# Kernel optimization log

Measured on AMD Instinct MI355X. Metric: run time of the kernel, lower is better.

Reference implementation:

```python
import jax, jax.numpy as jnp
import numpy as np

VOCAB = 50257
H = 512  # output_size == embed dim == lstm hidden
N = 65536  # number of tokens


def setup_inputs() -> dict:
    key = jax.random.key(0)
    ks = jax.random.split(key, 12)
    s = 1.0 / np.sqrt(H)  # torch LSTM/Linear init scale
    inp = {
        "ids": jax.random.randint(ks[0], (N,), 0, VOCAB, dtype=jnp.int64)
        if jax.config.jax_enable_x64 else jax.random.randint(ks[0], (N,), 0, VOCAB, dtype=jnp.int32),
        "emb": jax.random.normal(ks[1], (VOCAB, H), dtype=jnp.float32),
        # LSTM layer 0 (gate order: i, f, g, o)
        "W_ih0": jax.random.uniform(ks[2], (4 * H, H), jnp.float32, -s, s),
        "W_hh0": jax.random.uniform(ks[3], (4 * H, H), jnp.float32, -s, s),
        "b_ih0": jax.random.uniform(ks[4], (4 * H,), jnp.float32, -s, s),
        "b_hh0": jax.random.uniform(ks[5], (4 * H,), jnp.float32, -s, s),
        # LSTM layer 1
        "W_ih1": jax.random.uniform(ks[6], (4 * H, H), jnp.float32, -s, s),
        "W_hh1": jax.random.uniform(ks[7], (4 * H, H), jnp.float32, -s, s),
        "b_ih1": jax.random.uniform(ks[8], (4 * H,), jnp.float32, -s, s),
        "b_hh1": jax.random.uniform(ks[9], (4 * H,), jnp.float32, -s, s),
        # final Linear
        "W_lin": jax.random.uniform(ks[10], (H, H), jnp.float32, -s, s),
        "b_lin": jax.random.uniform(ks[11], (H,), jnp.float32, -s, s),
    }
    return inp


def _lstm_cell_zero_state(x, W_ih, b_ih, b_hh):
    # Single LSTM step with h_prev = c_prev = 0, so W_hh @ h_prev == 0.
    # gates: [N, 4H] in torch order i, f, g, o
    gates = x @ W_ih.T + (b_ih + b_hh)
    i, f, g, o = jnp.split(gates, 4, axis=-1)
    c = jax.nn.sigmoid(i) * jnp.tanh(g)  # f * c_prev == 0
    h = jax.nn.sigmoid(o) * jnp.tanh(c)
    return h


def reference(ids, emb, W_ih0, W_hh0, b_ih0, b_hh0, W_ih1, W_hh1, b_ih1, b_hh1, W_lin, b_lin):
    # Each token is processed with a fresh zero LSTM state, so the python
    # loop in the original vectorizes exactly over the token dim.
    x = emb[ids]                                   # [N, H]
    h0 = _lstm_cell_zero_state(x, W_ih0, b_ih0, b_hh0)   # layer 1 hidden
    h1 = _lstm_cell_zero_state(h0, W_ih1, b_ih1, b_hh1)  # layer 2 hidden (hidden[-1])
    out = jax.nn.relu(h1 @ W_lin.T + b_lin)        # [N, H]
    return out[:, None, :]                         # stacked [N, 1, H] like torch.stack of [1,H]
```

## Files before the change

kernel.cpp:

```cpp
#include <hip/hip_runtime.h>
#include <stdint.h>


typedef _Float16 half8 __attribute__((ext_vector_type(8)));
typedef __attribute__((ext_vector_type(4))) float float4v;
typedef __attribute__((ext_vector_type(4))) unsigned int uint4v;

__device__ __forceinline__ float sigmoidf_(float x) { return 1.0f / (1.0f + __expf(-x)); }
__device__ __forceinline__ float tanhf_(float x) { return 1.0f - 2.0f / (__expf(2.0f * x) + 1.0f); }

__device__ __forceinline__ void gl2lds16(const void* g, void* l) {
  __builtin_amdgcn_global_load_lds(
      (const __attribute__((address_space(1))) void*)g,
      (__attribute__((address_space(3))) void*)l, 16, 0, 0);
}

__global__ __launch_bounds__(256) void prep_kernel(
    const float* __restrict__ emb,
    const float* __restrict__ W0, const float* __restrict__ bi0, const float* __restrict__ bh0,
    const float* __restrict__ W1, const float* __restrict__ bi1, const float* __restrict__ bh1,
    const float* __restrict__ WL,
    _Float16* __restrict__ Ef,
    _Float16* __restrict__ W0f, _Float16* __restrict__ W1f, _Float16* __restrict__ WLf,
    float* __restrict__ b0p, float* __restrict__ b1p)
{
  int id = blockIdx.x * 256 + threadIdx.x;
  if (id < 3216448) {
    const float* s = emb + (size_t)id * 8;
    float4v v0 = *(const float4v*)s;
    float4v v1 = *(const float4v*)(s + 4);
    union { _Float16 h[8]; uint4v u; } P;
#pragma unroll
    for (int e = 0; e < 4; ++e) { P.h[e] = (_Float16)v0[e]; P.h[4 + e] = (_Float16)v1[e]; }
    *(uint4v*)(Ef + (size_t)id * 8) = P.u;
  } else if (id < 3347520) {
    int u = id - 3216448;
    int np = u >> 6, k0 = (u & 63) << 3;
    int n = ((np & 3) << 9) | (np >> 2);
    const float* s = W0 + n * 512 + k0;
    float4v v0 = *(const float4v*)s;
    float4v v1 = *(const float4v*)(s + 4);
    union { _Float16 h[8]; uint4v u; } P;
#pragma unroll
    for (int e = 0; e < 4; ++e) { P.h[e] = (_Float16)v0[e]; P.h[4 + e] = (_Float16)v1[e]; }
    *(uint4v*)(W0f + np * 512 + k0) = P.u;
  } else if (id < 3478592) {
    int u = id - 3347520;
    int np = u >> 6, k0 = (u & 63) << 3;
    int n = ((np & 3) << 9) | (np >> 2);
    const float* s = W1 + n * 512 + k0;
    float4v v0 = *(const float4v*)s;
    float4v v1 = *(const float4v*)(s + 4);
    union { _Float16 h[8]; uint4v u; } P;
#pragma unroll
    for (int e = 0; e < 4; ++e) { P.h[e] = (_Float16)v0[e]; P.h[4 + e] = (_Float16)v1[e]; }
    *(uint4v*)(W1f + np * 512 + k0) = P.u;
  } else if (id < 3511360) {
    int u = id - 3478592;
    const float* s = WL + (size_t)u * 8;
    float4v v0 = *(const float4v*)s;
    float4v v1 = *(const float4v*)(s + 4);
    union { _Float16 h[8]; uint4v u8; } P;
#pragma unroll
    for (int e = 0; e < 4; ++e) { P.h[e] = (_Float16)v0[e]; P.h[4 + e] = (_Float16)v1[e]; }
    *(uint4v*)(WLf + (size_t)u * 8) = P.u8;
  } else if (id < 3513408) {
    int np = id - 3511360;
    int n = ((np & 3) << 9) | (np >> 2);
    b0p[np] = bi0[n] + bh0[n];
  } else if (id < 3515456) {
    int np = id - 3513408;
    int n = ((np & 3) << 9) | (np >> 2);
    b1p[np] = bi1[n] + bh1[n];
  } else if (id < 3526656) {
    int u = id - 3515456;
    *(uint4v*)(Ef + 25731584 + (size_t)u * 8) = (uint4v){0u, 0u, 0u, 0u};
  }
}

template <int MODE>
__global__ __launch_bounds__(512, 4) void gemm_kernel(
    const _Float16* __restrict__ A, const int* __restrict__ ids,
    const _Float16* __restrict__ B, const float* __restrict__ bias,
    _Float16* __restrict__ Of, float* __restrict__ Out,
    int nbShift, int nbMask)
{
  __shared__ __align__(16) char smem[24576];
  _Float16* sA = (_Float16*)smem;
  _Float16* sB = (_Float16*)(smem + 16384);

  const int T = threadIdx.x;
  const int lane = T & 63;
  const int wv = T >> 6;
  const int wrow = wv >> 1, wcol = wv & 1;
  const int nwg = (int)gridDim.x;
  const int bid = (int)blockIdx.x;
  const int swz = (bid & 7) * (nwg >> 3) + (bid >> 3);
  const int mb = swz >> nbShift;
  const int nb = swz & nbMask;
  const size_t t0 = (size_t)mb * 256;
  const int n0 = nb * 128;

  const int r0 = T >> 2;
  const int qg = (T & 3) ^ ((r0 >> 1) & 3);
  size_t sr0 = t0 + r0, sr1 = t0 + 128 + r0;
  if (ids) { sr0 = (size_t)(unsigned)ids[sr0]; sr1 = (size_t)(unsigned)ids[sr1]; }
  const _Float16* gA0 = A + sr0 * 512 + qg * 8;
  const _Float16* gA1 = A + sr1 * 512 + qg * 8;
  const _Float16* gB  = B + (size_t)(n0 + r0) * 512 + qg * 8;

  const int m_ = lane & 15, qf = lane >> 4;
  const int qs = qf ^ ((m_ >> 1) & 3);
  const int offA = wrow * 2048 + m_ * 32 + qs * 8;
  const int offB = wcol * 2048 + m_ * 32 + qs * 8;

  float4v acc[4][4];
#pragma unroll
  for (int i = 0; i < 4; ++i)
#pragma unroll
    for (int j = 0; j < 4; ++j)
      acc[i][j] = (float4v){0.f, 0.f, 0.f, 0.f};

  for (int it = 0; it < 16; ++it) {
    gl2lds16(gA0, sA + T * 8);
    gl2lds16(gA1, sA + 4096 + T * 8);
    gl2lds16(gB,  sB + T * 8);
    gA0 += 32; gA1 += 32; gB += 32;
    __syncthreads();

    half8 a[4], b[4];
#pragma unroll
    for (int i = 0; i < 4; ++i) {
      a[i] = *(const half8*)(sA + offA + i * 512);
      b[i] = *(const half8*)(sB + offB + i * 512);
    }
#pragma unroll
    for (int i = 0; i < 4; ++i)
#pragma unroll
      for (int j = 0; j < 4; ++j)
        acc[i][j] = __builtin_amdgcn_mfma_f32_16x16x32_f16(b[j], a[i], acc[i][j], 0, 0, 0);
    __syncthreads();
  }

  float4v bq[4];
#pragma unroll
  for (int j = 0; j < 4; ++j)
    bq[j] = *(const float4v*)(bias + n0 + wcol * 64 + j * 16 + qf * 4);

  if (MODE == 0) {
    _Float16* hT = (_Float16*)smem;
    const int ub = wcol * 16 + qf;
#pragma unroll
    for (int i = 0; i < 4; ++i) {
      const int trow = wrow * 64 + i * 16 + m_;
#pragma unroll
      for (int j = 0; j < 4; ++j) {
        float yi = acc[i][j][0] + bq[j][0];
        float yg = acc[i][j][2] + bq[j][2];
        float yo = acc[i][j][3] + bq[j][3];
        float cc = sigmoidf_(yi) * tanhf_(yg);
        float hh = sigmoidf_(yo) * tanhf_(cc);
        hT[trow * 40 + ub + j * 4] = (_Float16)hh;
      }
    }
    __syncthreads();
    const int tl = T >> 1, hf = T & 1;
    const _Float16* src = hT + tl * 40 + hf * 16;
    uint4v v0 = *(const uint4v*)(src);
    uint4v v1 = *(const uint4v*)(src + 8);
    _Float16* dst = Of + (t0 + tl) * 512 + (size_t)(nb * 32) + hf * 16;
    *(uint4v*)dst = v0;
    *(uint4v*)(dst + 8) = v1;
  } else {
#pragma unroll
    for (int i = 0; i < 4; ++i) {
      const size_t row = t0 + wrow * 64 + i * 16 + m_;
#pragma unroll
      for (int j = 0; j < 4; ++j) {
        float4v v;
#pragma unroll
        for (int r2 = 0; r2 < 4; ++r2)
          v[r2] = fmaxf(acc[i][j][r2] + bq[j][r2], 0.0f);
        *(float4v*)(Out + row * 512 + (size_t)(n0 + wcol * 64 + j * 16 + qf * 4)) = v;
      }
    }
  }
}

extern "C" void kernel_launch(void* const* d_in, const int* in_sizes, int n_in,
                              void* d_out, int out_size, void* d_ws, size_t ws_size,
                              hipStream_t stream) {
  (void)in_sizes; (void)n_in; (void)out_size; (void)ws_size;
  const int*   ids   = (const int*)d_in[0];
  const float* emb   = (const float*)d_in[1];
  const float* W0    = (const float*)d_in[2];
  const float* bi0   = (const float*)d_in[4];
  const float* bh0   = (const float*)d_in[5];
  const float* W1    = (const float*)d_in[6];
  const float* bi1   = (const float*)d_in[8];
  const float* bh1   = (const float*)d_in[9];
  const float* WL    = (const float*)d_in[10];
  const float* blin  = (const float*)d_in[11];
  float* out = (float*)d_out;

  char* ws = (char*)d_ws;
  const size_t MB = 1024 * 1024;
  _Float16* W0f = (_Float16*)(ws);
  _Float16* W1f = (_Float16*)(ws + 2 * MB);
  _Float16* WLf = (_Float16*)(ws + 4 * MB);
  float*    b0p = (float*)(ws + 4 * MB + 512 * 1024);
  float*    b1p = (float*)(ws + 4 * MB + 512 * 1024 + 8192);
  _Float16* Ef  = (_Float16*)(ws + 8 * MB);
  _Float16* H1f = Ef;
  _Float16* H0f = (_Float16*)(ws + 72 * MB);

  prep_kernel<<<13776, 256, 0, stream>>>(emb, W0, bi0, bh0, W1, bi1, bh1, WL,
                                         Ef, W0f, W1f, WLf, b0p, b1p);
  gemm_kernel<0><<<3152, 512, 0, stream>>>(Ef, nullptr, W0f, b0p, H0f, nullptr, 4, 15);
  gemm_kernel<0><<<3152, 512, 0, stream>>>(H0f, nullptr, W1f, b1p, H1f, nullptr, 4, 15);
  gemm_kernel<1><<<1024, 512, 0, stream>>>(H1f, ids, WLf, blin, nullptr, out, 2, 3);
}
```

Baseline: 590.7 us.

## Double-buffer LDS tiles in the GEMM K-loop to overlap loads with MFMA

The K-loop now prefetches the next 32-wide K slice of A and B into a second LDS buffer while MFMAs run on the current one. Explicit vmcnt waits and raw s_barrier calls replace the two __syncthreads per iteration. The goal is to hide global-to-LDS load latency behind tensor-core work. In exchange, the static LDS allocation grows from 24 KB to 64 KB per block, which lowers how many 512-thread blocks fit on a CU and may cut latency hiding from occupancy.

```diff
diff --git a/kernel.cpp b/kernel.cpp
--- a/kernel.cpp
+++ b/kernel.cpp
@@ -85,10 +85,7 @@
     _Float16* __restrict__ Of, float* __restrict__ Out,
     int nbShift, int nbMask)
 {
-  __shared__ __align__(16) char smem[24576];
-  _Float16* sA = (_Float16*)smem;
-  _Float16* sB = (_Float16*)(smem + 16384);
-
+  __shared__ __align__(16) char smem[65536];
   const int T = threadIdx.x;
   const int lane = T & 63;
   const int wv = T >> 6;
@@ -109,10 +106,17 @@
   const _Float16* gA1 = A + sr1 * 512 + qg * 8;
   const _Float16* gB  = B + (size_t)(n0 + r0) * 512 + qg * 8;
 
+  const int d0 = T * 16;
+#define STAGE(dst) do { \
+    gl2lds16(gA0, (dst) + d0); \
+    gl2lds16(gA1, (dst) + 8192 + d0); \
+    gl2lds16(gB,  (dst) + 16384 + d0); \
+    gA0 += 32; gA1 += 32; gB += 32; } while (0)
+
   const int m_ = lane & 15, qf = lane >> 4;
   const int qs = qf ^ ((m_ >> 1) & 3);
   const int offA = wrow * 2048 + m_ * 32 + qs * 8;
-  const int offB = wcol * 2048 + m_ * 32 + qs * 8;
+  const int offB = 8192 + wcol * 2048 + m_ * 32 + qs * 8;
 
   float4v acc[4][4];
 #pragma unroll
@@ -121,26 +125,38 @@
     for (int j = 0; j < 4; ++j)
       acc[i][j] = (float4v){0.f, 0.f, 0.f, 0.f};
 
+  char* bufc = smem;
+  char* bufn = smem + 32768;
+  STAGE(bufc);
+
   for (int it = 0; it < 16; ++it) {
-    gl2lds16(gA0, sA + T * 8);
-    gl2lds16(gA1, sA + 4096 + T * 8);
-    gl2lds16(gB,  sB + T * 8);
-    gA0 += 32; gA1 += 32; gB += 32;
-    __syncthreads();
-
+    if (it < 15) {
+      STAGE(bufn);
+      asm volatile("s_waitcnt vmcnt(3)" ::: "memory");
+    } else {
+      asm volatile("s_waitcnt vmcnt(0)" ::: "memory");
+    }
+    __builtin_amdgcn_sched_barrier(0);
+    __builtin_amdgcn_s_barrier();
+
+    const _Float16* cur = (const _Float16*)bufc;
     half8 a[4], b[4];
 #pragma unroll
     for (int i = 0; i < 4; ++i) {
-      a[i] = *(const half8*)(sA + offA + i * 512);
-      b[i] = *(const half8*)(sB + offB + i * 512);
+      a[i] = *(const half8*)(cur + offA + i * 512);
+      b[i] = *(const half8*)(cur + offB + i * 512);
     }
 #pragma unroll
     for (int i = 0; i < 4; ++i)
 #pragma unroll
       for (int j = 0; j < 4; ++j)
         acc[i][j] = __builtin_amdgcn_mfma_f32_16x16x32_f16(b[j], a[i], acc[i][j], 0, 0, 0);
-    __syncthreads();
+    __builtin_amdgcn_sched_barrier(0);
+    __builtin_amdgcn_s_barrier();
+    __builtin_amdgcn_sched_barrier(0);
+    char* tc = bufc; bufc = bufn; bufn = tc;
   }
+#undef STAGE
 
   float4v bq[4];
 #pragma unroll
```

Result: faster. 541.1 us (-8.4%).
